# Kernel tuning notes

Measured on AMD Instinct MI355X. Metric: run time of the kernel, lower is better.

The kernel has to match this reference:

```python
import jax, jax.numpy as jnp
import numpy as np

N_NODES = 50000
N_EDGES = 800000
IN_CH = 128
HID = 64
PROJ = 32


def _gcn_norm(edge_index, n):
    # add self loops, symmetric normalization D^-1/2 (A+I) D^-1/2
    loop = jnp.arange(n, dtype=edge_index.dtype)
    src = jnp.concatenate([edge_index[0], loop])
    dst = jnp.concatenate([edge_index[1], loop])
    deg = jax.ops.segment_sum(jnp.ones_like(dst, jnp.float32), dst, num_segments=n)
    dinv = deg ** -0.5  # deg >= 1 due to self loops
    norm = dinv[src] * dinv[dst]
    return src, dst, norm


def _propagate(h, src, dst, norm, n):
    # gather -> scale -> scatter-add (message passing along A_hat)
    return jax.ops.segment_sum(h[src] * norm[:, None], dst, num_segments=n)


def _ho_gcn_layer(x, src, dst, norm, Ws, b, n):
    # out = sum_{k=1..max_order} (A_hat^k x) W_k + b
    out = jnp.zeros((n, Ws[0].shape[1]), x.dtype)
    h = x
    for W in Ws:
        h = _propagate(h, src, dst, norm, n)
        out = out + h @ W
    return out + b


def setup_inputs() -> dict:
    key = jax.random.key(0)
    ks = jax.random.split(key, 16)

    def w(k, fan_in, fan_out):
        return (jax.random.normal(k, (fan_in, fan_out), jnp.float32) / np.sqrt(fan_in)).astype(jnp.float32)

    x = jax.random.normal(ks[0], (N_NODES, IN_CH), jnp.float32)
    edge_index = jax.random.randint(ks[1], (2, N_EDGES), 0, N_NODES, dtype=jnp.int64)
    return {
        "x": x,
        "edge_index": edge_index,
        # conv1: max_order=2 -> two weights
        "W1_1": w(ks[2], IN_CH, HID), "W1_2": w(ks[3], IN_CH, HID),
        "b1": jnp.zeros((HID,), jnp.float32),
        # conv2
        "W2_1": w(ks[4], HID, HID // 2), "W2_2": w(ks[5], HID, HID // 2),
        "b2": jnp.zeros((HID // 2,), jnp.float32),
        # projection head
        "Wp1": w(ks[6], HID // 2, PROJ), "bp1": jnp.zeros((PROJ,), jnp.float32),
        "Wp2": w(ks[7], PROJ, PROJ), "bp2": jnp.zeros((PROJ,), jnp.float32),
        # coordinate head
        "Wc1": w(ks[8], HID // 2, HID // 4), "bc1": jnp.zeros((HID // 4,), jnp.float32),
        "Wc2": w(ks[9], HID // 4, 2), "bc2": jnp.zeros((2,), jnp.float32),
    }


def reference(x, edge_index, W1_1, W1_2, b1, W2_1, W2_2, b2,
              Wp1, bp1, Wp2, bp2, Wc1, bc1, Wc2, bc2):
    n = x.shape[0]
    src, dst, norm = _gcn_norm(edge_index, n)
    h1 = jax.nn.relu(_ho_gcn_layer(x, src, dst, norm, (W1_1, W1_2), b1, n))
    # dropout is identity in eval/reference mode
    h2 = jax.nn.relu(_ho_gcn_layer(h1, src, dst, norm, (W2_1, W2_2), b2, n))
    z = jax.nn.relu(h2 @ Wp1 + bp1) @ Wp2 + bp2
    coordinates = jax.nn.relu(h2 @ Wc1 + bc1) @ Wc2 + bc2
    return (coordinates, z)
```

## Files before the change

kernel.cpp:

```cpp
#include <hip/hip_runtime.h>

#define NN 50000
#define NE 800000
#define S 4
#define BINW 12500
#define NN4 (NN * S)
#define NBLK2 ((NN4 + 255) / 256)

__global__ __launch_bounds__(256) void zero_cnt_k(int* __restrict__ cnt) {
    int i = blockIdx.x * blockDim.x + threadIdx.x;
    if (i < NN4) cnt[i] = 0;
}

__global__ __launch_bounds__(256) void hist_k(const int* __restrict__ src,
                                              const int* __restrict__ dst,
                                              int* __restrict__ cnt,
                                              int* __restrict__ rank) {
    int e = blockIdx.x * blockDim.x + threadIdx.x;
    if (e >= NE) return;
    int s = src[e], d = dst[e];
    int b = s / BINW;
    rank[e] = atomicAdd(&cnt[d * S + b], 1);
}

__global__ __launch_bounds__(256) void sum_blocks_k(const int* __restrict__ cnt,
                                                    int* __restrict__ bsum,
                                                    float* __restrict__ dinv) {
    __shared__ int s[256];
    int t = threadIdx.x;
    int i = blockIdx.x * 256 + t;
    int v = (i < NN4) ? cnt[i] : 0;
    s[t] = v;
    if (i < NN4 && (i & 3) == 0) {
        int deg = cnt[i] + cnt[i + 1] + cnt[i + 2] + cnt[i + 3];
        dinv[i >> 2] = rsqrtf((float)(deg + 1));
    }
    __syncthreads();
    for (int off = 128; off > 0; off >>= 1) {
        if (t < off) s[t] += s[t + off];
        __syncthreads();
    }
    if (t == 0) bsum[blockIdx.x] = s[0];
}

__global__ __launch_bounds__(1024) void scan_blocks_k(int* __restrict__ bsum,
                                                      int* __restrict__ rowsS) {
    __shared__ int s[1024];
    int t = threadIdx.x;
    int v = (t < NBLK2) ? bsum[t] : 0;
    s[t] = v;
    __syncthreads();
    for (int off = 1; off < 1024; off <<= 1) {
        int x = (t >= off) ? s[t - off] : 0;
        __syncthreads();
        s[t] += x;
        __syncthreads();
    }
    if (t < NBLK2) bsum[t] = s[t] - v;
    if (t == 0) rowsS[NN4] = NE;
}

__global__ __launch_bounds__(256) void scan_final_k(const int* __restrict__ cnt,
                                                    const int* __restrict__ bsum,
                                                    int* __restrict__ rowsS) {
    __shared__ int s[256];
    int t = threadIdx.x;
    int i = blockIdx.x * 256 + t;
    int v = (i < NN4) ? cnt[i] : 0;
    s[t] = v;
    __syncthreads();
    for (int off = 1; off < 256; off <<= 1) {
        int x = (t >= off) ? s[t - off] : 0;
        __syncthreads();
        s[t] += x;
        __syncthreads();
    }
    if (i < NN4) rowsS[i] = bsum[blockIdx.x] + s[t] - v;
}

__global__ __launch_bounds__(256) void scatter_k(const int* __restrict__ src,
                                                 const int* __restrict__ dst,
                                                 const int* __restrict__ rank,
                                                 const int* __restrict__ rowsS,
                                                 int* __restrict__ col) {
    int e = blockIdx.x * blockDim.x + threadIdx.x;
    if (e >= NE) return;
    int s = src[e], d = dst[e];
    int b = s / BINW;
    col[rowsS[d * S + b] + rank[e]] = s;
}

template<int LOG2C4, bool ADDIN>
__global__ __launch_bounds__(256) void prop_k(const float4* __restrict__ h4,
                                              const float4* __restrict__ addin4,
                                              const float* __restrict__ bias,
                                              float4* __restrict__ out4,
                                              const int* __restrict__ rowsS,
                                              const int* __restrict__ col,
                                              const float* __restrict__ dinv) {
    const int C4 = 1 << LOG2C4;
    unsigned tid = blockIdx.x * blockDim.x + threadIdx.x;
    unsigned node = tid >> LOG2C4;
    if (node >= NN) return;
    unsigned lane = tid & (C4 - 1);
    size_t rowoff = ((size_t)node << LOG2C4) + lane;
    float dn = dinv[node];
    float w0 = dn * dn;
    float4 hv = h4[rowoff];
    float4 acc;
    if (ADDIN) {
        float4 a = addin4[rowoff];
        acc.x = a.x + w0 * hv.x; acc.y = a.y + w0 * hv.y;
        acc.z = a.z + w0 * hv.z; acc.w = a.w + w0 * hv.w;
    } else {
        float4 b = ((const float4*)bias)[lane];
        acc.x = b.x + w0 * hv.x; acc.y = b.y + w0 * hv.y;
        acc.z = b.z + w0 * hv.z; acc.w = b.w + w0 * hv.w;
    }
    int base = node * S;
    int rs = rowsS[base];
#pragma unroll
    for (int p = 1; p <= S; p++) {
        int re = rowsS[base + p];
        int i = rs;
        for (; i + 4 <= re; i += 4) {
            int c0 = col[i + 0];
            int c1 = col[i + 1];
            int c2 = col[i + 2];
            int c3 = col[i + 3];
            float4 v0 = h4[((size_t)c0 << LOG2C4) + lane];
            float4 v1 = h4[((size_t)c1 << LOG2C4) + lane];
            float4 v2 = h4[((size_t)c2 << LOG2C4) + lane];
            float4 v3 = h4[((size_t)c3 << LOG2C4) + lane];
            float a0 = dinv[c0] * dn;
            float a1 = dinv[c1] * dn;
            float a2 = dinv[c2] * dn;
            float a3 = dinv[c3] * dn;
            acc.x += a0 * v0.x + a1 * v1.x + a2 * v2.x + a3 * v3.x;
            acc.y += a0 * v0.y + a1 * v1.y + a2 * v2.y + a3 * v3.y;
            acc.z += a0 * v0.z + a1 * v1.z + a2 * v2.z + a3 * v3.z;
            acc.w += a0 * v0.w + a1 * v1.w + a2 * v2.w + a3 * v3.w;
        }
        for (; i < re; i++) {
            int c = col[i];
            float4 v = h4[((size_t)c << LOG2C4) + lane];
            float w = dinv[c] * dn;
            acc.x += w * v.x; acc.y += w * v.y; acc.z += w * v.z; acc.w += w * v.w;
        }
        rs = re;
    }
    if (!ADDIN) {
        acc.x = fmaxf(acc.x, 0.0f); acc.y = fmaxf(acc.y, 0.0f);
        acc.z = fmaxf(acc.z, 0.0f); acc.w = fmaxf(acc.w, 0.0f);
    }
    out4[rowoff] = acc;
}

__global__ __launch_bounds__(256) void gemm1_k(const float* __restrict__ A,
                                               const float* __restrict__ WA,
                                               const float* __restrict__ WB,
                                               float* __restrict__ outA,
                                               float* __restrict__ outB, int n) {
    __shared__ float As[64 * 68];
    __shared__ float W1s[64 * 68];
    __shared__ float W2s[64 * 68];
    const int t = threadIdx.x;
    const int tj = t & 15;
    const int tn = t >> 4;
    const int n0 = blockIdx.x * 64;
    float acc[4][8] = {};

    for (int kc = 0; kc < 128; kc += 64) {
        if (kc) __syncthreads();
        {
            int idx = t;
#pragma unroll
            for (int r = 0; r < 4; r++, idx += 256) {
                int nl = idx >> 4, q = idx & 15;
                int node = n0 + nl; node = node < n ? node : n - 1;
                float4 a = ((const float4*)A)[(size_t)node * 32 + (kc >> 2) + q];
                *(float4*)&As[nl * 68 + q * 4] = a;
            }
        }
        {
            int idx = t;
#pragma unroll
            for (int r = 0; r < 4; r++, idx += 256) {
                int kl = idx >> 4, j4 = idx & 15;
                *(float4*)&W1s[kl * 68 + j4 * 4] = ((const float4*)WA)[(size_t)(kc + kl) * 16 + j4];
                *(float4*)&W2s[kl * 68 + j4 * 4] = ((const float4*)WB)[(size_t)(kc + kl) * 16 + j4];
            }
        }
        __syncthreads();

        const float* ap = &As[tn * 4 * 68];
        const float* w1p = &W1s[tj * 4];
        const float* w2p = &W2s[tj * 4];
#pragma unroll 2
        for (int k4 = 0; k4 < 16; k4++) {
            float4 a0 = *(const float4*)&ap[0 * 68 + k4 * 4];
            float4 a1 = *(const float4*)&ap[1 * 68 + k4 * 4];
            float4 a2 = *(const float4*)&ap[2 * 68 + k4 * 4];
            float4 a3 = *(const float4*)&ap[3 * 68 + k4 * 4];
#pragma unroll
            for (int kk = 0; kk < 4; kk++) {
                float4 w1 = *(const float4*)&w1p[(k4 * 4 + kk) * 68];
                float4 w2 = *(const float4*)&w2p[(k4 * 4 + kk) * 68];
                float av0 = kk == 0 ? a0.x : kk == 1 ? a0.y : kk == 2 ? a0.z : a0.w;
                float av1 = kk == 0 ? a1.x : kk == 1 ? a1.y : kk == 2 ? a1.z : a1.w;
                float av2 = kk == 0 ? a2.x : kk == 1 ? a2.y : kk == 2 ? a2.z : a2.w;
                float av3 = kk == 0 ? a3.x : kk == 1 ? a3.y : kk == 2 ? a3.z : a3.w;
#define FMA8(m, AV)                                                     \
                acc[m][0] += AV * w1.x; acc[m][1] += AV * w1.y;          \
                acc[m][2] += AV * w1.z; acc[m][3] += AV * w1.w;          \
                acc[m][4] += AV * w2.x; acc[m][5] += AV * w2.y;          \
                acc[m][6] += AV * w2.z; acc[m][7] += AV * w2.w;
                FMA8(0, av0)
                FMA8(1, av1)
                FMA8(2, av2)
                FMA8(3, av3)
#undef FMA8
            }
        }
    }

#pragma unroll
    for (int m = 0; m < 4; m++) {
        int node = n0 + tn * 4 + m;
        if (node < n) {
            *(float4*)&outA[(size_t)node * 64 + tj * 4] =
                make_float4(acc[m][0], acc[m][1], acc[m][2], acc[m][3]);
            *(float4*)&outB[(size_t)node * 64 + tj * 4] =
                make_float4(acc[m][4], acc[m][5], acc[m][6], acc[m][7]);
        }
    }
}

template<int K, int JW>
__global__ __launch_bounds__(256) void gemm_k(const float* __restrict__ A,
                                              const float* __restrict__ WA,
                                              const float* __restrict__ WB,
                                              float* __restrict__ out, int n) {
    __shared__ float As[64 * 68];
    __shared__ float Ws[64 * 68];
    const int t = threadIdx.x;
    const int tj = t & 15;
    const int tn = t >> 4;
    const int n0 = blockIdx.x * 64;
    float acc[4][4] = {};

    for (int kc = 0; kc < K; kc += 64) {
        if (kc) __syncthreads();
        {
            int idx = t;
#pragma unroll
            for (int r = 0; r < 4; r++, idx += 256) {
                int nl = idx >> 4, q = idx & 15;
                int node = n0 + nl; node = node < n ? node : n - 1;
                float4 a = ((const float4*)A)[(size_t)node * (K / 4) + (kc >> 2) + q];
                *(float4*)&As[nl * 68 + q * 4] = a;
            }
        }
        {
            int idx = t;
#pragma unroll
            for (int r = 0; r < 4; r++, idx += 256) {
                int kl = idx >> 4, j4 = idx & 15;
                const float* W = (j4 < 8) ? WA : WB;
                float4 w = ((const float4*)W)[(size_t)(kc + kl) * 8 + (j4 & 7)];
                *(float4*)&Ws[kl * 68 + j4 * 4] = w;
            }
        }
        __syncthreads();

        const float* ap = &As[tn * 4 * 68];
        const float* wp = &Ws[tj * 4];
#pragma unroll 4
        for (int k4 = 0; k4 < 16; k4++) {
            float4 a0 = *(const float4*)&ap[0 * 68 + k4 * 4];
            float4 a1 = *(const float4*)&ap[1 * 68 + k4 * 4];
            float4 a2 = *(const float4*)&ap[2 * 68 + k4 * 4];
            float4 a3 = *(const float4*)&ap[3 * 68 + k4 * 4];
            float4 w0 = *(const float4*)&wp[(k4 * 4 + 0) * 68];
            float4 w1 = *(const float4*)&wp[(k4 * 4 + 1) * 68];
            float4 w2 = *(const float4*)&wp[(k4 * 4 + 2) * 68];
            float4 w3 = *(const float4*)&wp[(k4 * 4 + 3) * 68];
#define FMA_ROW(m, AV)                                                   \
            acc[m][0] += AV.x * w0.x + AV.y * w1.x + AV.z * w2.x + AV.w * w3.x; \
            acc[m][1] += AV.x * w0.y + AV.y * w1.y + AV.z * w2.y + AV.w * w3.y; \
            acc[m][2] += AV.x * w0.z + AV.y * w1.z + AV.z * w2.z + AV.w * w3.z; \
            acc[m][3] += AV.x * w0.w + AV.y * w1.w + AV.z * w2.w + AV.w * w3.w;
            FMA_ROW(0, a0)
            FMA_ROW(1, a1)
            FMA_ROW(2, a2)
            FMA_ROW(3, a3)
#undef FMA_ROW
        }
    }

    int mat = tj >> 3;
    int jw = (tj & 7) * 4;
    float* ob = out + (size_t)mat * n * JW + jw;
#pragma unroll
    for (int m = 0; m < 4; m++) {
        int node = n0 + tn * 4 + m;
        if (node < n)
            *(float4*)&ob[(size_t)node * JW] =
                make_float4(acc[m][0], acc[m][1], acc[m][2], acc[m][3]);
    }
}

__global__ __launch_bounds__(256) void heads_k(const float* __restrict__ h2,
                                               const float* __restrict__ Wp1, const float* __restrict__ bp1,
                                               const float* __restrict__ Wp2, const float* __restrict__ bp2,
                                               const float* __restrict__ Wc1, const float* __restrict__ bc1,
                                               const float* __restrict__ Wc2, const float* __restrict__ bc2,
                                               float* __restrict__ coord, float* __restrict__ z, int n) {
    __shared__ float sWp1[32 * 32], sWp2[32 * 32], sWc1[32 * 16], sWc2[32];
    __shared__ float sbp1[32], sbp2[32], sbc1[16], sbc2[2];
    __shared__ float sh[32 * 36], st[32 * 36], stc[32 * 18];
    const int t = threadIdx.x;
    for (int i = t; i < 1024; i += 256) { sWp1[i] = Wp1[i]; sWp2[i] = Wp2[i]; }
    for (int i = t; i < 512; i += 256) sWc1[i] = Wc1[i];
    if (t < 32) { sWc2[t] = Wc2[t]; sbp1[t] = bp1[t]; sbp2[t] = bp2[t]; }
    if (t < 16) sbc1[t] = bc1[t];
    if (t < 2) sbc2[t] = bc2[t];

    const int n0 = blockIdx.x * 32;
    const int nl = t >> 3;
    const int jq = t & 7;
    const int node = n0 + nl;
    {
        float4 v = make_float4(0.f, 0.f, 0.f, 0.f);
        if (node < n) v = *(const float4*)&h2[(size_t)node * 32 + jq * 4];
        *(float4*)&sh[nl * 36 + jq * 4] = v;
    }
    __syncthreads();

    float4 a = *(const float4*)&sbp1[jq * 4];
#pragma unroll
    for (int k = 0; k < 32; k++) {
        float hv = sh[nl * 36 + k];
        float4 w = *(const float4*)&sWp1[k * 32 + jq * 4];
        a.x += hv * w.x; a.y += hv * w.y; a.z += hv * w.z; a.w += hv * w.w;
    }
    a.x = fmaxf(a.x, 0.f); a.y = fmaxf(a.y, 0.f);
    a.z = fmaxf(a.z, 0.f); a.w = fmaxf(a.w, 0.f);
    *(float4*)&st[nl * 36 + jq * 4] = a;

    float2 c = *(const float2*)&sbc1[jq * 2];
#pragma unroll
    for (int k = 0; k < 32; k++) {
        float hv = sh[nl * 36 + k];
        float2 w = *(const float2*)&sWc1[k * 16 + jq * 2];
        c.x += hv * w.x; c.y += hv * w.y;
    }
    c.x = fmaxf(c.x, 0.f); c.y = fmaxf(c.y, 0.f);
    *(float2*)&stc[nl * 18 + jq * 2] = c;
    __syncthreads();

    float4 zz = *(const float4*)&sbp2[jq * 4];
#pragma unroll
    for (int k = 0; k < 32; k++) {
        float tv = st[nl * 36 + k];
        float4 w = *(const float4*)&sWp2[k * 32 + jq * 4];
        zz.x += tv * w.x; zz.y += tv * w.y; zz.z += tv * w.z; zz.w += tv * w.w;
    }
    if (node < n) *(float4*)&z[(size_t)node * 32 + jq * 4] = zz;

    if (jq < 2) {
        float s = sbc2[jq];
#pragma unroll
        for (int k = 0; k < 16; k++) s += stc[nl * 18 + k] * sWc2[k * 2 + jq];
        if (node < n) coord[(size_t)node * 2 + jq] = s;
    }
}

extern "C" void kernel_launch(void* const* d_in, const int* in_sizes, int n_in,
                              void* d_out, int out_size, void* d_ws, size_t ws_size,
                              hipStream_t stream) {
    const float* x    = (const float*)d_in[0];
    const int*   ei   = (const int*)d_in[1];
    const int*   src  = ei;
    const int*   dst  = ei + NE;
    const float* W1_1 = (const float*)d_in[2];
    const float* W1_2 = (const float*)d_in[3];
    const float* b1   = (const float*)d_in[4];
    const float* W2_1 = (const float*)d_in[5];
    const float* W2_2 = (const float*)d_in[6];
    const float* b2   = (const float*)d_in[7];
    const float* Wp1  = (const float*)d_in[8];
    const float* bp1  = (const float*)d_in[9];
    const float* Wp2  = (const float*)d_in[10];
    const float* bp2  = (const float*)d_in[11];
    const float* Wc1  = (const float*)d_in[12];
    const float* bc1  = (const float*)d_in[13];
    const float* Wc2  = (const float*)d_in[14];
    const float* bc2  = (const float*)d_in[15];

    float* ws    = (float*)d_ws;
    float* dinv  = ws;
    int*   cnt   = (int*)(dinv + NN);
    int*   rowsS = cnt + NN4;
    int*   bsum  = rowsS + NN4 + 4;
    int*   rank  = bsum + 1024;
    int*   col   = rank + NE;
    float* bufY  = (float*)(col + NE);
    float* bufZ  = bufY + (size_t)NN * 128;

    float* y1 = bufY;
    float* y2 = bufY + (size_t)NN * 64;
    float* u  = y1;
    float* h1 = y2;
    float* z1 = bufZ;
    float* z2 = bufZ + (size_t)NN * 32;
    float* u2 = z1;
    float* h2 = z2;

    float* coord = (float*)d_out;
    float* z     = (float*)d_out + 2 * NN;

    zero_cnt_k<<<NBLK2, 256, 0, stream>>>(cnt);
    hist_k<<<(NE + 255) / 256, 256, 0, stream>>>(src, dst, cnt, rank);
    sum_blocks_k<<<NBLK2, 256, 0, stream>>>(cnt, bsum, dinv);
    scan_blocks_k<<<1, 1024, 0, stream>>>(bsum, rowsS);
    scan_final_k<<<NBLK2, 256, 0, stream>>>(cnt, bsum, rowsS);
    scatter_k<<<(NE + 255) / 256, 256, 0, stream>>>(src, dst, rank, rowsS, col);

    gemm1_k<<<(NN + 63) / 64, 256, 0, stream>>>(x, W1_1, W1_2, y1, y2, NN);
    prop_k<4, true><<<(NN * 16 + 255) / 256, 256, 0, stream>>>(
        (const float4*)y2, (const float4*)y1, nullptr, (float4*)u, rowsS, col, dinv);
    prop_k<4, false><<<(NN * 16 + 255) / 256, 256, 0, stream>>>(
        (const float4*)u, nullptr, b1, (float4*)h1, rowsS, col, dinv);
    gemm_k<64, 32><<<(NN + 63) / 64, 256, 0, stream>>>(h1, W2_1, W2_2, bufZ, NN);
    prop_k<3, true><<<(NN * 8 + 255) / 256, 256, 0, stream>>>(
        (const float4*)z2, (const float4*)z1, nullptr, (float4*)u2, rowsS, col, dinv);
    prop_k<3, false><<<(NN * 8 + 255) / 256, 256, 0, stream>>>(
        (const float4*)u2, nullptr, b2, (float4*)h2, rowsS, col, dinv);
    heads_k<<<(NN + 31) / 32, 256, 0, stream>>>(h2, Wp1, bp1, Wp2, bp2, Wc1, bc1, Wc2, bc2, coord, z, NN);
}
```

Baseline: 320.5 us.

## Pad CSR rows to multiples of four and precompute per-edge source weights

The CSR build now pads each node's row to a multiple of four entries with zero-weight dummy edges, and the scatter kernel also writes a per-edge weight array holding dinv[src]. The propagation kernel then runs a single loop over the padded row using int4/float4 vector loads of column indices and weights, software-prefetching the next group. It no longer reads dinv per neighbor and no longer needs the per-bin inner loops with scalar tails. The cost is extra workspace, a little padding traffic, and wasted gathers of row 0 for padded slots.

Result: slower. 332.5 us (+3.8%).

```diff
diff --git a/kernel.cpp b/kernel.cpp
--- a/kernel.cpp
+++ b/kernel.cpp
@@ -6,6 +6,7 @@
 #define BINW 12500
 #define NN4 (NN * S)
 #define NBLK2 ((NN4 + 255) / 256)
+#define NEP (NE + 3 * NN + 8)
 
 __global__ __launch_bounds__(256) void zero_cnt_k(int* __restrict__ cnt) {
     int i = blockIdx.x * blockDim.x + threadIdx.x;
@@ -29,12 +30,19 @@
     __shared__ int s[256];
     int t = threadIdx.x;
     int i = blockIdx.x * 256 + t;
-    int v = (i < NN4) ? cnt[i] : 0;
+    int v = 0;
+    if (i < NN4) {
+        v = cnt[i];
+        if ((i & 3) == 0) {
+            int deg = cnt[i] + cnt[i + 1] + cnt[i + 2] + cnt[i + 3];
+            dinv[i >> 2] = rsqrtf((float)(deg + 1));
+        }
+        if ((i & 3) == 3) {
+            int deg = cnt[i - 3] + cnt[i - 2] + cnt[i - 1] + cnt[i];
+            v += (4 - (deg & 3)) & 3;
+        }
+    }
     s[t] = v;
-    if (i < NN4 && (i & 3) == 0) {
-        int deg = cnt[i] + cnt[i + 1] + cnt[i + 2] + cnt[i + 3];
-        dinv[i >> 2] = rsqrtf((float)(deg + 1));
-    }
     __syncthreads();
     for (int off = 128; off > 0; off >>= 1) {
         if (t < off) s[t] += s[t + off];
@@ -57,7 +65,7 @@
         __syncthreads();
     }
     if (t < NBLK2) bsum[t] = s[t] - v;
-    if (t == 0) rowsS[NN4] = NE;
+    if (t == NBLK2 - 1) rowsS[NN4] = s[t];
 }
 
 __global__ __launch_bounds__(256) void scan_final_k(const int* __restrict__ cnt,
@@ -66,7 +74,14 @@
     __shared__ int s[256];
     int t = threadIdx.x;
     int i = blockIdx.x * 256 + t;
-    int v = (i < NN4) ? cnt[i] : 0;
+    int v = 0;
+    if (i < NN4) {
+        v = cnt[i];
+        if ((i & 3) == 3) {
+            int deg = cnt[i - 3] + cnt[i - 2] + cnt[i - 1] + cnt[i];
+            v += (4 - (deg & 3)) & 3;
+        }
+    }
     s[t] = v;
     __syncthreads();
     for (int off = 1; off < 256; off <<= 1) {
@@ -82,12 +97,26 @@
                                                  const int* __restrict__ dst,
                                                  const int* __restrict__ rank,
                                                  const int* __restrict__ rowsS,
-                                                 int* __restrict__ col) {
+                                                 const int* __restrict__ cnt,
+                                                 const float* __restrict__ dinv,
+                                                 int* __restrict__ col,
+                                                 float* __restrict__ wv) {
     int e = blockIdx.x * blockDim.x + threadIdx.x;
-    if (e >= NE) return;
-    int s = src[e], d = dst[e];
-    int b = s / BINW;
-    col[rowsS[d * S + b] + rank[e]] = s;
+    if (e < NE) {
+        int s = src[e], d = dst[e];
+        int b = s / BINW;
+        int pos = rowsS[d * S + b] + rank[e];
+        col[pos] = s;
+        wv[pos] = dinv[s];
+    } else {
+        int node = e - NE;
+        if (node < NN) {
+            int i3 = node * S + (S - 1);
+            int end = rowsS[i3] + cnt[i3];
+            int nxt = rowsS[i3 + 1];
+            for (int i = end; i < nxt; i++) { col[i] = 0; wv[i] = 0.0f; }
+        }
+    }
 }
 
 template<int LOG2C4, bool ADDIN>
@@ -97,6 +126,7 @@
                                               float4* __restrict__ out4,
                                               const int* __restrict__ rowsS,
                                               const int* __restrict__ col,
+                                              const float* __restrict__ wv,
                                               const float* __restrict__ dinv) {
     const int C4 = 1 << LOG2C4;
     unsigned tid = blockIdx.x * blockDim.x + threadIdx.x;
@@ -105,53 +135,40 @@
     unsigned lane = tid & (C4 - 1);
     size_t rowoff = ((size_t)node << LOG2C4) + lane;
     float dn = dinv[node];
+    float4 hv = h4[rowoff];
+    int rs = rowsS[node << 2];
+    int re = rowsS[(node << 2) + 4];
+    int4 c = *(const int4*)(col + rs);
+    float4 w = *(const float4*)(wv + rs);
+    float4 g = make_float4(0.f, 0.f, 0.f, 0.f);
+    for (int i = rs; i < re; i += 4) {
+        int4 cc = c;
+        float4 wc = w;
+        c = *(const int4*)(col + i + 4);
+        w = *(const float4*)(wv + i + 4);
+        float4 v0 = h4[((size_t)(unsigned)cc.x << LOG2C4) + lane];
+        float4 v1 = h4[((size_t)(unsigned)cc.y << LOG2C4) + lane];
+        float4 v2 = h4[((size_t)(unsigned)cc.z << LOG2C4) + lane];
+        float4 v3 = h4[((size_t)(unsigned)cc.w << LOG2C4) + lane];
+        g.x += wc.x * v0.x + wc.y * v1.x + wc.z * v2.x + wc.w * v3.x;
+        g.y += wc.x * v0.y + wc.y * v1.y + wc.z * v2.y + wc.w * v3.y;
+        g.z += wc.x * v0.z + wc.y * v1.z + wc.z * v2.z + wc.w * v3.z;
+        g.w += wc.x * v0.w + wc.y * v1.w + wc.z * v2.w + wc.w * v3.w;
+    }
     float w0 = dn * dn;
-    float4 hv = h4[rowoff];
     float4 acc;
     if (ADDIN) {
         float4 a = addin4[rowoff];
-        acc.x = a.x + w0 * hv.x; acc.y = a.y + w0 * hv.y;
-        acc.z = a.z + w0 * hv.z; acc.w = a.w + w0 * hv.w;
+        acc.x = a.x + w0 * hv.x + dn * g.x;
+        acc.y = a.y + w0 * hv.y + dn * g.y;
+        acc.z = a.z + w0 * hv.z + dn * g.z;
+        acc.w = a.w + w0 * hv.w + dn * g.w;
     } else {
         float4 b = ((const float4*)bias)[lane];
-        acc.x = b.x + w0 * hv.x; acc.y = b.y + w0 * hv.y;
-        acc.z = b.z + w0 * hv.z; acc.w = b.w + w0 * hv.w;
-    }
-    int base = node * S;
-    int rs = rowsS[base];
-#pragma unroll
-    for (int p = 1; p <= S; p++) {
-        int re = rowsS[base + p];
-        int i = rs;
-        for (; i + 4 <= re; i += 4) {
-            int c0 = col[i + 0];
-            int c1 = col[i + 1];
-            int c2 = col[i + 2];
-            int c3 = col[i + 3];
-            float4 v0 = h4[((size_t)c0 << LOG2C4) + lane];
-            float4 v1 = h4[((size_t)c1 << LOG2C4) + lane];
-            float4 v2 = h4[((size_t)c2 << LOG2C4) + lane];
-            float4 v3 = h4[((size_t)c3 << LOG2C4) + lane];
-            float a0 = dinv[c0] * dn;
-            float a1 = dinv[c1] * dn;
-            float a2 = dinv[c2] * dn;
-            float a3 = dinv[c3] * dn;
-            acc.x += a0 * v0.x + a1 * v1.x + a2 * v2.x + a3 * v3.x;
-            acc.y += a0 * v0.y + a1 * v1.y + a2 * v2.y + a3 * v3.y;
-            acc.z += a0 * v0.z + a1 * v1.z + a2 * v2.z + a3 * v3.z;
-            acc.w += a0 * v0.w + a1 * v1.w + a2 * v2.w + a3 * v3.w;
-        }
-        for (; i < re; i++) {
-            int c = col[i];
-            float4 v = h4[((size_t)c << LOG2C4) + lane];
-            float w = dinv[c] * dn;
-            acc.x += w * v.x; acc.y += w * v.y; acc.z += w * v.z; acc.w += w * v.w;
-        }
-        rs = re;
-    }
-    if (!ADDIN) {
-        acc.x = fmaxf(acc.x, 0.0f); acc.y = fmaxf(acc.y, 0.0f);
-        acc.z = fmaxf(acc.z, 0.0f); acc.w = fmaxf(acc.w, 0.0f);
+        acc.x = fmaxf(b.x + w0 * hv.x + dn * g.x, 0.0f);
+        acc.y = fmaxf(b.y + w0 * hv.y + dn * g.y, 0.0f);
+        acc.z = fmaxf(b.z + w0 * hv.z + dn * g.z, 0.0f);
+        acc.w = fmaxf(b.w + w0 * hv.w + dn * g.w, 0.0f);
     }
     out4[rowoff] = acc;
 }
@@ -405,7 +422,8 @@
     int*   bsum  = rowsS + NN4 + 4;
     int*   rank  = bsum + 1024;
     int*   col   = rank + NE;
-    float* bufY  = (float*)(col + NE);
+    float* wv    = (float*)(col + NEP);
+    float* bufY  = wv + NEP;
     float* bufZ  = bufY + (size_t)NN * 128;
 
     float* y1 = bufY;
@@ -425,17 +443,17 @@
     sum_blocks_k<<<NBLK2, 256, 0, stream>>>(cnt, bsum, dinv);
     scan_blocks_k<<<1, 1024, 0, stream>>>(bsum, rowsS);
     scan_final_k<<<NBLK2, 256, 0, stream>>>(cnt, bsum, rowsS);
-    scatter_k<<<(NE + 255) / 256, 256, 0, stream>>>(src, dst, rank, rowsS, col);
+    scatter_k<<<(NE + NN + 255) / 256, 256, 0, stream>>>(src, dst, rank, rowsS, cnt, dinv, col, wv);
 
     gemm1_k<<<(NN + 63) / 64, 256, 0, stream>>>(x, W1_1, W1_2, y1, y2, NN);
     prop_k<4, true><<<(NN * 16 + 255) / 256, 256, 0, stream>>>(
-        (const float4*)y2, (const float4*)y1, nullptr, (float4*)u, rowsS, col, dinv);
+        (const float4*)y2, (const float4*)y1, nullptr, (float4*)u, rowsS, col, wv, dinv);
     prop_k<4, false><<<(NN * 16 + 255) / 256, 256, 0, stream>>>(
-        (const float4*)u, nullptr, b1, (float4*)h1, rowsS, col, dinv);
+        (const float4*)u, nullptr, b1, (float4*)h1, rowsS, col, wv, dinv);
     gemm_k<64, 32><<<(NN + 63) / 64, 256, 0, stream>>>(h1, W2_1, W2_2, bufZ, NN);
     prop_k<3, true><<<(NN * 8 + 255) / 256, 256, 0, stream>>>(
-        (const float4*)z2, (const float4*)z1, nullptr, (float4*)u2, rowsS, col, dinv);
+        (const float4*)z2, (const float4*)z1, nullptr, (float4*)u2, rowsS, col, wv, dinv);
     prop_k<3, false><<<(NN * 8 + 255) / 256, 256, 0, stream>>>(
-        (const float4*)u2, nullptr, b2, (float4*)h2, rowsS, col, dinv);
+        (const float4*)u2, nullptr, b2, (float4*)h2, rowsS, col, wv, dinv);
     heads_k<<<(NN + 31) / 32, 256, 0, stream>>>(h2, Wp1, bp1, Wp2, bp2, Wc1, bc1, Wc2, bc2, coord, z, NN);
 }
```

## Fuse first GEMM with edge histogram and fold block-sum scan into final scan

Applied to the files above, without the earlier changes.

Runs the first layer's dense GEMM and the edge-count histogram in one launch by splitting the grid, so the histogram atomics and GEMM compute can share the device. Shrinks the GEMM K-chunk from 64 to 32 to cut shared memory per block. Removes the single-block scan kernel: each final-scan block now sums the preceding block totals itself. This saves two launches and the serial one-block step, but adds redundant per-block prefix work over roughly 800 totals.

Result: faster. 297.1 us (-7.3%).

```diff
diff --git a/kernel.cpp b/kernel.cpp
--- a/kernel.cpp
+++ b/kernel.cpp
@@ -6,21 +6,106 @@
 #define BINW 12500
 #define NN4 (NN * S)
 #define NBLK2 ((NN4 + 255) / 256)
+#define NBG ((NN + 63) / 64)
+#define NBH ((NE + 255) / 256)
 
 __global__ __launch_bounds__(256) void zero_cnt_k(int* __restrict__ cnt) {
     int i = blockIdx.x * blockDim.x + threadIdx.x;
     if (i < NN4) cnt[i] = 0;
 }
 
-__global__ __launch_bounds__(256) void hist_k(const int* __restrict__ src,
-                                              const int* __restrict__ dst,
-                                              int* __restrict__ cnt,
-                                              int* __restrict__ rank) {
-    int e = blockIdx.x * blockDim.x + threadIdx.x;
-    if (e >= NE) return;
-    int s = src[e], d = dst[e];
-    int b = s / BINW;
-    rank[e] = atomicAdd(&cnt[d * S + b], 1);
+__global__ __launch_bounds__(256) void gemm1_hist_k(const float* __restrict__ A,
+                                                    const float* __restrict__ WA,
+                                                    const float* __restrict__ WB,
+                                                    float* __restrict__ outA,
+                                                    float* __restrict__ outB,
+                                                    const int* __restrict__ src,
+                                                    const int* __restrict__ dst,
+                                                    int* __restrict__ cnt,
+                                                    int* __restrict__ rank) {
+    if (blockIdx.x >= NBG) {
+        int e = (blockIdx.x - NBG) * 256 + threadIdx.x;
+        if (e < NE) {
+            int s = src[e], d = dst[e];
+            int b = s / BINW;
+            rank[e] = atomicAdd(&cnt[d * S + b], 1);
+        }
+        return;
+    }
+
+    __shared__ float As[64 * 36];
+    __shared__ float W1s[32 * 68];
+    __shared__ float W2s[32 * 68];
+    const int t = threadIdx.x;
+    const int tj = t & 15;
+    const int tn = t >> 4;
+    const int n0 = blockIdx.x * 64;
+    float acc[4][8] = {};
+
+    for (int kc = 0; kc < 128; kc += 32) {
+        if (kc) __syncthreads();
+        {
+            int idx = t;
+#pragma unroll
+            for (int r = 0; r < 2; r++, idx += 256) {
+                int nl = idx >> 3, q = idx & 7;
+                int node = n0 + nl; node = node < NN ? node : NN - 1;
+                float4 a = ((const float4*)A)[(size_t)node * 32 + (kc >> 2) + q];
+                *(float4*)&As[nl * 36 + q * 4] = a;
+            }
+        }
+        {
+            int idx = t;
+#pragma unroll
+            for (int r = 0; r < 2; r++, idx += 256) {
+                int kl = idx >> 4, j4 = idx & 15;
+                *(float4*)&W1s[kl * 68 + j4 * 4] = ((const float4*)WA)[(size_t)(kc + kl) * 16 + j4];
+                *(float4*)&W2s[kl * 68 + j4 * 4] = ((const float4*)WB)[(size_t)(kc + kl) * 16 + j4];
+            }
+        }
+        __syncthreads();
+
+        const float* ap = &As[tn * 4 * 36];
+        const float* w1p = &W1s[tj * 4];
+        const float* w2p = &W2s[tj * 4];
+#pragma unroll 2
+        for (int k4 = 0; k4 < 8; k4++) {
+            float4 a0 = *(const float4*)&ap[0 * 36 + k4 * 4];
+            float4 a1 = *(const float4*)&ap[1 * 36 + k4 * 4];
+            float4 a2 = *(const float4*)&ap[2 * 36 + k4 * 4];
+            float4 a3 = *(const float4*)&ap[3 * 36 + k4 * 4];
+#pragma unroll
+            for (int kk = 0; kk < 4; kk++) {
+                float4 w1 = *(const float4*)&w1p[(k4 * 4 + kk) * 68];
+                float4 w2 = *(const float4*)&w2p[(k4 * 4 + kk) * 68];
+                float av0 = kk == 0 ? a0.x : kk == 1 ? a0.y : kk == 2 ? a0.z : a0.w;
+                float av1 = kk == 0 ? a1.x : kk == 1 ? a1.y : kk == 2 ? a1.z : a1.w;
+                float av2 = kk == 0 ? a2.x : kk == 1 ? a2.y : kk == 2 ? a2.z : a2.w;
+                float av3 = kk == 0 ? a3.x : kk == 1 ? a3.y : kk == 2 ? a3.z : a3.w;
+#define FMA8(m, AV)                                                     \
+                acc[m][0] += AV * w1.x; acc[m][1] += AV * w1.y;          \
+                acc[m][2] += AV * w1.z; acc[m][3] += AV * w1.w;          \
+                acc[m][4] += AV * w2.x; acc[m][5] += AV * w2.y;          \
+                acc[m][6] += AV * w2.z; acc[m][7] += AV * w2.w;
+                FMA8(0, av0)
+                FMA8(1, av1)
+                FMA8(2, av2)
+                FMA8(3, av3)
+#undef FMA8
+            }
+        }
+    }
+
+#pragma unroll
+    for (int m = 0; m < 4; m++) {
+        int node = n0 + tn * 4 + m;
+        if (node < NN) {
+            *(float4*)&outA[(size_t)node * 64 + tj * 4] =
+                make_float4(acc[m][0], acc[m][1], acc[m][2], acc[m][3]);
+            *(float4*)&outB[(size_t)node * 64 + tj * 4] =
+                make_float4(acc[m][4], acc[m][5], acc[m][6], acc[m][7]);
+        }
+    }
 }
 
 __global__ __launch_bounds__(256) void sum_blocks_k(const int* __restrict__ cnt,
@@ -43,28 +128,23 @@
     if (t == 0) bsum[blockIdx.x] = s[0];
 }
 
-__global__ __launch_bounds__(1024) void scan_blocks_k(int* __restrict__ bsum,
-                                                      int* __restrict__ rowsS) {
-    __shared__ int s[1024];
-    int t = threadIdx.x;
-    int v = (t < NBLK2) ? bsum[t] : 0;
-    s[t] = v;
-    __syncthreads();
-    for (int off = 1; off < 1024; off <<= 1) {
-        int x = (t >= off) ? s[t - off] : 0;
-        __syncthreads();
-        s[t] += x;
-        __syncthreads();
-    }
-    if (t < NBLK2) bsum[t] = s[t] - v;
-    if (t == 0) rowsS[NN4] = NE;
-}
-
 __global__ __launch_bounds__(256) void scan_final_k(const int* __restrict__ cnt,
                                                     const int* __restrict__ bsum,
                                                     int* __restrict__ rowsS) {
+    __shared__ int sOff[256];
     __shared__ int s[256];
     int t = threadIdx.x;
+    int accum = 0;
+    for (int idx = t; idx < NBLK2; idx += 256)
+        if (idx < blockIdx.x) accum += bsum[idx];
+    sOff[t] = accum;
+    __syncthreads();
+    for (int off = 128; off > 0; off >>= 1) {
+        if (t < off) sOff[t] += sOff[t + off];
+        __syncthreads();
+    }
+    int boff = sOff[0];
+
     int i = blockIdx.x * 256 + t;
     int v = (i < NN4) ? cnt[i] : 0;
     s[t] = v;
@@ -75,7 +155,8 @@
         s[t] += x;
         __syncthreads();
     }
-    if (i < NN4) rowsS[i] = bsum[blockIdx.x] + s[t] - v;
+    if (i < NN4) rowsS[i] = boff + s[t] - v;
+    if (blockIdx.x == 0 && t == 0) rowsS[NN4] = NE;
 }
 
 __global__ __launch_bounds__(256) void scatter_k(const int* __restrict__ src,
@@ -156,86 +237,6 @@
     out4[rowoff] = acc;
 }
 
-__global__ __launch_bounds__(256) void gemm1_k(const float* __restrict__ A,
-                                               const float* __restrict__ WA,
-                                               const float* __restrict__ WB,
-                                               float* __restrict__ outA,
-                                               float* __restrict__ outB, int n) {
-    __shared__ float As[64 * 68];
-    __shared__ float W1s[64 * 68];
-    __shared__ float W2s[64 * 68];
-    const int t = threadIdx.x;
-    const int tj = t & 15;
-    const int tn = t >> 4;
-    const int n0 = blockIdx.x * 64;
-    float acc[4][8] = {};
-
-    for (int kc = 0; kc < 128; kc += 64) {
-        if (kc) __syncthreads();
-        {
-            int idx = t;
-#pragma unroll
-            for (int r = 0; r < 4; r++, idx += 256) {
-                int nl = idx >> 4, q = idx & 15;
-                int node = n0 + nl; node = node < n ? node : n - 1;
-                float4 a = ((const float4*)A)[(size_t)node * 32 + (kc >> 2) + q];
-                *(float4*)&As[nl * 68 + q * 4] = a;
-            }
-        }
-        {
-            int idx = t;
-#pragma unroll
-            for (int r = 0; r < 4; r++, idx += 256) {
-                int kl = idx >> 4, j4 = idx & 15;
-                *(float4*)&W1s[kl * 68 + j4 * 4] = ((const float4*)WA)[(size_t)(kc + kl) * 16 + j4];
-                *(float4*)&W2s[kl * 68 + j4 * 4] = ((const float4*)WB)[(size_t)(kc + kl) * 16 + j4];
-            }
-        }
-        __syncthreads();
-
-        const float* ap = &As[tn * 4 * 68];
-        const float* w1p = &W1s[tj * 4];
-        const float* w2p = &W2s[tj * 4];
-#pragma unroll 2
-        for (int k4 = 0; k4 < 16; k4++) {
-            float4 a0 = *(const float4*)&ap[0 * 68 + k4 * 4];
-            float4 a1 = *(const float4*)&ap[1 * 68 + k4 * 4];
-            float4 a2 = *(const float4*)&ap[2 * 68 + k4 * 4];
-            float4 a3 = *(const float4*)&ap[3 * 68 + k4 * 4];
-#pragma unroll
-            for (int kk = 0; kk < 4; kk++) {
-                float4 w1 = *(const float4*)&w1p[(k4 * 4 + kk) * 68];
-                float4 w2 = *(const float4*)&w2p[(k4 * 4 + kk) * 68];
-                float av0 = kk == 0 ? a0.x : kk == 1 ? a0.y : kk == 2 ? a0.z : a0.w;
-                float av1 = kk == 0 ? a1.x : kk == 1 ? a1.y : kk == 2 ? a1.z : a1.w;
-                float av2 = kk == 0 ? a2.x : kk == 1 ? a2.y : kk == 2 ? a2.z : a2.w;
-                float av3 = kk == 0 ? a3.x : kk == 1 ? a3.y : kk == 2 ? a3.z : a3.w;
-#define FMA8(m, AV)                                                     \
-                acc[m][0] += AV * w1.x; acc[m][1] += AV * w1.y;          \
-                acc[m][2] += AV * w1.z; acc[m][3] += AV * w1.w;          \
-                acc[m][4] += AV * w2.x; acc[m][5] += AV * w2.y;          \
-                acc[m][6] += AV * w2.z; acc[m][7] += AV * w2.w;
-                FMA8(0, av0)
-                FMA8(1, av1)
-                FMA8(2, av2)
-                FMA8(3, av3)
-#undef FMA8
-            }
-        }
-    }
-
-#pragma unroll
-    for (int m = 0; m < 4; m++) {
-        int node = n0 + tn * 4 + m;
-        if (node < n) {
-            *(float4*)&outA[(size_t)node * 64 + tj * 4] =
-                make_float4(acc[m][0], acc[m][1], acc[m][2], acc[m][3]);
-            *(float4*)&outB[(size_t)node * 64 + tj * 4] =
-                make_float4(acc[m][4], acc[m][5], acc[m][6], acc[m][7]);
-        }
-    }
-}
-
 template<int K, int JW>
 __global__ __launch_bounds__(256) void gemm_k(const float* __restrict__ A,
                                               const float* __restrict__ WA,
@@ -421,13 +422,12 @@
     float* z     = (float*)d_out + 2 * NN;
 
     zero_cnt_k<<<NBLK2, 256, 0, stream>>>(cnt);
-    hist_k<<<(NE + 255) / 256, 256, 0, stream>>>(src, dst, cnt, rank);
+    gemm1_hist_k<<<NBG + NBH, 256, 0, stream>>>(x, W1_1, W1_2, y1, y2,
+                                                src, dst, cnt, rank);
     sum_blocks_k<<<NBLK2, 256, 0, stream>>>(cnt, bsum, dinv);
-    scan_blocks_k<<<1, 1024, 0, stream>>>(bsum, rowsS);
     scan_final_k<<<NBLK2, 256, 0, stream>>>(cnt, bsum, rowsS);
     scatter_k<<<(NE + 255) / 256, 256, 0, stream>>>(src, dst, rank, rowsS, col);
 
-    gemm1_k<<<(NN + 63) / 64, 256, 0, stream>>>(x, W1_1, W1_2, y1, y2, NN);
     prop_k<4, true><<<(NN * 16 + 255) / 256, 256, 0, stream>>>(
         (const float4*)y2, (const float4*)y1, nullptr, (float4*)u, rowsS, col, dinv);
     prop_k<4, false><<<(NN * 16 + 255) / 256, 256, 0, stream>>>(
```
